# Kernel optimization log

Hardware: AMD Instinct MI355X
Metric: run time of the kernel (lower is better)

Reference implementation:

```python
import jax, jax.numpy as jnp
import numpy as np

B_, C_, T_, F_ = 1, 64, 256, 128
D_CONV, D_STATE, DT_RANK = 4, 16, 4
D_INNER = 2 * C_
EPS = 1e-5


def setup_inputs():
    key = jax.random.key(0)
    ks = jax.random.split(key, 12)
    s = 0.05
    return {
        'x': jax.random.normal(ks[0], (B_, C_, T_, F_), jnp.float32),
        'norm_w': jnp.ones((4, C_), jnp.float32),
        'in_proj_w': jax.random.normal(ks[1], (4, 2 * D_INNER, C_), jnp.float32) * s,
        'conv_w': jax.random.normal(ks[2], (4, D_INNER, 1, D_CONV), jnp.float32) * 0.3,
        'conv_b': jnp.zeros((4, D_INNER), jnp.float32),
        'x_proj_w': jax.random.normal(ks[3], (4, DT_RANK + 2 * D_STATE, D_INNER), jnp.float32) * s,
        'dt_proj_w': jax.random.normal(ks[4], (4, D_INNER, DT_RANK), jnp.float32) * 0.1,
        'dt_proj_b': jnp.log(jnp.expm1(jax.random.uniform(ks[5], (4, D_INNER), jnp.float32, 1e-3, 0.1))),
        'A_log': jnp.log(jax.random.uniform(ks[6], (4, D_INNER, D_STATE), jnp.float32, 0.5, 16.0)),
        'Dp': jnp.ones((4, D_INNER), jnp.float32),
        'out_proj_w': jax.random.normal(ks[7], (4, C_, D_INNER), jnp.float32) * s,
        'tlin_w': jax.random.normal(ks[8], (2 * C_, C_), jnp.float32) * s,
        'tlin_b': jnp.zeros((C_,), jnp.float32),
        'flin_w': jax.random.normal(ks[9], (2 * C_, C_), jnp.float32) * s,
        'flin_b': jnp.zeros((C_,), jnp.float32),
    }


def _rmsnorm(x, w):
    return x * jax.lax.rsqrt(jnp.mean(x * x, axis=-1, keepdims=True) + EPS) * w


def _mamba(u, p):
    # u: (N, L, d_model) ; selective-scan Mamba mixer
    N, L, _ = u.shape
    xz = jnp.einsum('nld,ed->nle', u, p['in_proj_w'])  # (N,L,2*di)
    x, z = jnp.split(xz, 2, axis=-1)
    # causal depthwise conv over time
    xT = jnp.swapaxes(x, 1, 2)  # (N, di, L)
    xc = jax.lax.conv_general_dilated(xT, p['conv_w'], (1,), [(D_CONV - 1, 0)],
                                      feature_group_count=D_INNER)
    x = jnp.swapaxes(jax.nn.silu(xc + p['conv_b'][None, :, None]), 1, 2)  # (N,L,di)
    xdbl = jnp.einsum('nld,ed->nle', x, p['x_proj_w'])
    dt, Bm, Cm = jnp.split(xdbl, [DT_RANK, DT_RANK + D_STATE], axis=-1)
    dt = jax.nn.softplus(jnp.einsum('nlr,dr->nld', dt, p['dt_proj_w']) + p['dt_proj_b'])
    A = -jnp.exp(p['A_log'])  # (di, ds)

    def step(h, inp):
        dt_t, B_t, C_t, x_t = inp  # (N,di),(N,ds),(N,ds),(N,di)
        dA = jnp.exp(dt_t[:, :, None] * A)  # (N,di,ds)
        h = dA * h + dt_t[:, :, None] * B_t[:, None, :] * x_t[:, :, None]
        return h, jnp.einsum('nds,ns->nd', h, C_t)

    h0 = jnp.zeros((N, D_INNER, D_STATE), u.dtype)
    _, ys = jax.lax.scan(step, h0, (jnp.swapaxes(dt, 0, 1), jnp.swapaxes(Bm, 0, 1),
                                    jnp.swapaxes(Cm, 0, 1), jnp.swapaxes(x, 0, 1)))
    y = jnp.swapaxes(ys, 0, 1) + x * p['Dp']
    y = y * jax.nn.silu(z)
    return jnp.einsum('nld,od->nlo', y, p['out_proj_w'])


def _block(u, p):
    # mamba Block with residual: out = mixer(rmsnorm(u)) + u
    return _mamba(_rmsnorm(u, p['norm_w']), p) + u


def _bimamba(u, pf, pb):
    yf = _block(u, pf)
    yb = jnp.flip(_block(jnp.flip(u, 1), pb), 1)
    return jnp.concatenate([yf, yb], axis=-1)


def _pick(i, norm_w, in_proj_w, conv_w, conv_b, x_proj_w, dt_proj_w, dt_proj_b, A_log, Dp, out_proj_w):
    return dict(norm_w=norm_w[i], in_proj_w=in_proj_w[i], conv_w=conv_w[i], conv_b=conv_b[i],
                x_proj_w=x_proj_w[i], dt_proj_w=dt_proj_w[i], dt_proj_b=dt_proj_b[i],
                A_log=A_log[i], Dp=Dp[i], out_proj_w=out_proj_w[i])


def _tfmamba(x, norm_w, in_proj_w, conv_w, conv_b, x_proj_w, dt_proj_w, dt_proj_b,
             A_log, Dp, out_proj_w, tlin_w, tlin_b, flin_w, flin_b):
    b, c, t, f = x.shape
    P = [_pick(i, norm_w, in_proj_w, conv_w, conv_b, x_proj_w, dt_proj_w, dt_proj_b, A_log, Dp, out_proj_w)
         for i in range(4)]
    # time axis
    xt = jnp.reshape(jnp.transpose(x, (0, 3, 2, 1)), (b * f, t, c))
    xt_out = _bimamba(xt, P[0], P[1])  # (b*f, t, 2c)
    xt = xt + jnp.einsum('nti,io->nto', xt_out, tlin_w) + tlin_b
    # frequency axis
    xf = jnp.reshape(jnp.transpose(jnp.reshape(xt, (b, f, t, c)), (0, 2, 1, 3)), (b * t, f, c))
    xf_out = _bimamba(xf, P[2], P[3])  # (b*t, f, 2c)
    xf = xf + jnp.einsum('nfi,io->nfo', xf_out, flin_w) + flin_b
    return jnp.transpose(jnp.reshape(xf, (b, t, f, c)), (0, 3, 1, 2))


def reference(x, norm_w, in_proj_w, conv_w, conv_b, x_proj_w, dt_proj_w, dt_proj_b,
              A_log, Dp, out_proj_w, tlin_w, tlin_b, flin_w, flin_b):
    return _tfmamba(x, norm_w, in_proj_w, conv_w, conv_b, x_proj_w, dt_proj_w, dt_proj_b,
                    A_log, Dp, out_proj_w, tlin_w, tlin_b, flin_w, flin_b)
```

## Files before the change

kernel.cpp:

```cpp
#include <hip/hip_runtime.h>
#include <math.h>

#define C_DIM 64
#define T_DIM 256
#define F_DIM 128
#define DI    128
#define DS    16
#define CK    16

typedef __attribute__((ext_vector_type(8))) short bf16x8;
typedef __attribute__((ext_vector_type(4))) float f32x4;

__device__ __forceinline__ float silu_f(float v){ return v / (1.0f + __expf(-v)); }

__device__ __forceinline__ unsigned short f2bf(float f){
  union{float f; unsigned u;} v; v.f = f;
  unsigned r = v.u + 0x7FFFu + ((v.u >> 16) & 1u);
  return (unsigned short)(r >> 16);
}

__device__ __forceinline__ int swz64(int row, int col){
  return row*64 + (col ^ ((row & 7) << 3));
}
__device__ __forceinline__ int swz128(int row, int col){
  return row*128 + (col ^ ((row & 7) << 3));
}

__global__ __launch_bounds__(256) void k_prep(const float* __restrict__ ipw,
                                              const float* __restrict__ opw,
                                              const float* __restrict__ xpw,
                                              const float* __restrict__ tlw,
                                              unsigned short* __restrict__ wbuf){
  const int i = blockIdx.x*256 + threadIdx.x;
  if(i < 65536){
    wbuf[i] = f2bf(ipw[i]);
  } else if(i < 98304){
    wbuf[i] = f2bf(opw[i - 65536]);
  } else if(i < 122880){
    const int j = i - 98304;
    const int p = j / 6144, rr = (j - p*6144) >> 7, k = j & 127;
    wbuf[i] = (rr < 36) ? f2bf(xpw[p*4608 + rr*128 + k]) : (unsigned short)0;
  } else {
    const int j = i - 122880;
    const int o = j >> 7, k = j & 127;
    wbuf[i] = f2bf(tlw[k*64 + o]);
  }
}

__global__ __launch_bounds__(256) void k_transpose_in(const float* __restrict__ x,
                                                      float* __restrict__ xt){
  __shared__ float tile[64][133];
  const int t = blockIdx.x;
  {
    const int fi = threadIdx.x & 127, cg = threadIdx.x >> 7;
    for(int c = cg*32; c < cg*32 + 32; ++c)
      tile[c][fi] = x[(size_t)c*32768 + (size_t)t*128 + fi];
  }
  __syncthreads();
  {
    const int ci = threadIdx.x & 63, fg = threadIdx.x >> 6;
    for(int f = fg*32; f < fg*32 + 32; ++f)
      xt[(size_t)f*16384 + (size_t)t*64 + ci] = tile[ci][f];
  }
}

__global__ __launch_bounds__(256, 3) void k_mamba(
    const float* __restrict__ src, int N, int L, long long sn, long long sl,
    int pbase,
    const float* __restrict__ norm_w,   const unsigned short* __restrict__ wbf,
    const float* __restrict__ conv_w,   const float* __restrict__ conv_b,
    const float* __restrict__ dt_proj_w,
    const float* __restrict__ dt_proj_b,const float* __restrict__ A_log,
    const float* __restrict__ Dp,       float* __restrict__ obuf)
{
  __shared__ __align__(16) unsigned short u_bf[CK*64];
  __shared__ float x_s[CK+3][132];
  __shared__ float z_s[CK][132];
  __shared__ float xc_s[CK][132];
  __shared__ __align__(16) unsigned short xc_bf[CK*128];
  __shared__ __align__(16) float dtr_s[CK][4];
  __shared__ __align__(16) float B_s[CK][20];
  __shared__ __align__(16) float C_s[CK][20];
  __shared__ __align__(16) unsigned short y_bf[CK*128];
  __shared__ float w_cv[512];
  __shared__ float b_cv[128];
  __shared__ float nw[64];

  const int tid = threadIdx.x;
  const int bid = blockIdx.x;
  const int dir = (bid >= N) ? 1 : 0;
  const int n   = dir ? (bid - N) : bid;
  const int p   = pbase + dir;

  const int lane = tid & 63;
  const int wv   = tid >> 6;
  const int fr   = lane & 15;
  const int fk   = (lane >> 4) << 3;

  for(int i = tid; i < 512; i += 256) w_cv[i] = conv_w[p*512 + i];
  if(tid < 128) b_cv[tid] = conv_b[p*128 + tid];
  if(tid < 64) nw[tid] = norm_w[p*64 + tid];
  for(int i = tid; i < 3*128; i += 256){ x_s[i >> 7][i & 127] = 0.0f; }

  const unsigned short* WinB  = wbf + (size_t)p*16384;
  const unsigned short* WoutB = wbf + 65536 + (size_t)p*8192;
  const unsigned short* XpB   = wbf + 98304 + (size_t)p*6144;
  bf16x8 aW[4][2];
  #pragma unroll
  for(int ot = 0; ot < 4; ++ot)
    #pragma unroll
    for(int kh = 0; kh < 2; ++kh)
      aW[ot][kh] = *(const bf16x8*)(WinB + (wv*64 + ot*16 + fr)*64 + kh*32 + fk);
  bf16x8 aO[4];
  #pragma unroll
  for(int kc = 0; kc < 4; ++kc)
    aO[kc] = *(const bf16x8*)(WoutB + (wv*16 + fr)*128 + kc*32 + fk);
  bf16x8 aXP[4];
  if(wv < 3){
    #pragma unroll
    for(int kc = 0; kc < 4; ++kc)
      aXP[kc] = *(const bf16x8*)(XpB + (wv*16 + fr)*128 + kc*32 + fk);
  }

  const int d_own = tid >> 1;
  const int sh    = (tid & 1) * 8;
  const int odd   = tid & 1;
  const float4 wdt4  = *(const float4*)(dt_proj_w + p*512 + d_own*4);
  const float  bdt_r = dt_proj_b[p*128 + d_own];
  const float  dvec_r= Dp[p*128 + d_own];
  float A_r[8], h[8];
  #pragma unroll
  for(int i = 0; i < 8; ++i){
    A_r[i] = -__expf(A_log[p*2048 + d_own*16 + sh + i]) * 1.44269504f;
    h[i] = 0.0f;
  }
  __syncthreads();

  for(int c0 = 0; c0 < L; c0 += CK){
    if(c0 > 0){
      for(int i = tid; i < 3*128; i += 256){
        int r = i >> 7, ch = i & 127;
        x_s[r][ch] = x_s[CK + r][ch];
      }
    }
    {
      const int g = tid >> 4, j = tid & 15, c4 = j*4;
      const int l = c0 + g;
      const int lo = dir ? (L - 1 - l) : l;
      const float4 v = *(const float4*)(src + (size_t)n*sn + (size_t)lo*sl + c4);
      float ssq = v.x*v.x + v.y*v.y + v.z*v.z + v.w*v.w;
      ssq += __shfl_xor(ssq, 1); ssq += __shfl_xor(ssq, 2);
      ssq += __shfl_xor(ssq, 4); ssq += __shfl_xor(ssq, 8);
      const float sc = rsqrtf(ssq * (1.0f/64.0f) + 1e-5f);
      ushort4 pk;
      pk.x = f2bf(v.x * sc * nw[c4+0]);
      pk.y = f2bf(v.y * sc * nw[c4+1]);
      pk.z = f2bf(v.z * sc * nw[c4+2]);
      pk.w = f2bf(v.w * sc * nw[c4+3]);
      *(ushort4*)&u_bf[swz64(g, c4)] = pk;
    }
    __syncthreads();

    {
      const bf16x8 b0 = *(const bf16x8*)&u_bf[swz64(fr, fk)];
      const bf16x8 b1 = *(const bf16x8*)&u_bf[swz64(fr, 32 + fk)];
      #pragma unroll
      for(int ot = 0; ot < 4; ++ot){
        f32x4 acc = {0.f, 0.f, 0.f, 0.f};
        acc = __builtin_amdgcn_mfma_f32_16x16x32_bf16(aW[ot][0], b0, acc, 0, 0, 0);
        acc = __builtin_amdgcn_mfma_f32_16x16x32_bf16(aW[ot][1], b1, acc, 0, 0, 0);
        const int ob = wv*64 + ot*16 + ((lane >> 4) << 2);
        if(wv < 2){
          #pragma unroll
          for(int r = 0; r < 4; ++r) x_s[3 + fr][ob + r] = acc[r];
        } else {
          #pragma unroll
          for(int r = 0; r < 4; ++r) z_s[fr][ob + r - 128] = acc[r];
        }
      }
    }
    __syncthreads();

    {
      const int g = tid >> 4, j = tid & 15;
      #pragma unroll
      for(int i = 0; i < 8; ++i){
        const int ch = j + 16*i;
        float a = b_cv[ch];
        a += w_cv[ch*4+0] * x_s[g+0][ch];
        a += w_cv[ch*4+1] * x_s[g+1][ch];
        a += w_cv[ch*4+2] * x_s[g+2][ch];
        a += w_cv[ch*4+3] * x_s[g+3][ch];
        const float s = silu_f(a);
        xc_s[g][ch] = s;
        xc_bf[swz128(g, ch)] = f2bf(s);
      }
    }
    __syncthreads();

    if(wv < 3){
      f32x4 acc = {0.f, 0.f, 0.f, 0.f};
      #pragma unroll
      for(int kc = 0; kc < 4; ++kc){
        const bf16x8 b = *(const bf16x8*)&xc_bf[swz128(fr, kc*32 + fk)];
        acc = __builtin_amdgcn_mfma_f32_16x16x32_bf16(aXP[kc], b, acc, 0, 0, 0);
      }
      const int ob36 = wv*16 + ((lane >> 4) << 2);
      #pragma unroll
      for(int r = 0; r < 4; ++r){
        const int o36 = ob36 + r;
        const float v = acc[r];
        if(o36 < 4)       dtr_s[fr][o36] = v;
        else if(o36 < 20) B_s[fr][o36 - 4] = v;
        else if(o36 < 36) C_s[fr][o36 - 20] = v;
      }
    }
    __syncthreads();

    {
      float my_dt[8];
      #pragma unroll
      for(int q = 0; q < 8; ++q){
        const int l = odd*8 + q;
        const float4 r4 = *(const float4*)&dtr_s[l][0];
        float a = bdt_r + wdt4.x*r4.x + wdt4.y*r4.y + wdt4.z*r4.z + wdt4.w*r4.w;
        my_dt[q] = fmaxf(a, 0.0f) + log1pf(__expf(-fabsf(a)));
      }
      float ot_dt[8];
      #pragma unroll
      for(int q = 0; q < 8; ++q) ot_dt[q] = __shfl_xor(my_dt[q], 1);
      #pragma unroll
      for(int l = 0; l < CK; ++l){
        const float dtv = ((l >> 3) == odd) ? my_dt[l & 7] : ot_dt[l & 7];
        const float xv  = xc_s[l][d_own];
        const float4 b0 = *(const float4*)&B_s[l][sh];
        const float4 b1 = *(const float4*)&B_s[l][sh + 4];
        const float4 g0 = *(const float4*)&C_s[l][sh];
        const float4 g1 = *(const float4*)&C_s[l][sh + 4];
        const float bb[8] = {b0.x,b0.y,b0.z,b0.w,b1.x,b1.y,b1.z,b1.w};
        const float cc[8] = {g0.x,g0.y,g0.z,g0.w,g1.x,g1.y,g1.z,g1.w};
        const float dx = dtv * xv;
        float yp = 0.0f;
        #pragma unroll
        for(int i = 0; i < 8; ++i){
          h[i] = exp2f(dtv * A_r[i]) * h[i] + dx * bb[i];
          yp += h[i] * cc[i];
        }
        const float yo = yp + __shfl_xor(yp, 1);
        if(odd == 0){
          const float zv = z_s[l][d_own];
          y_bf[swz128(l, d_own)] = f2bf((yo + xv * dvec_r) * silu_f(zv));
        }
      }
    }
    __syncthreads();

    {
      f32x4 acc = {0.f, 0.f, 0.f, 0.f};
      #pragma unroll
      for(int kc = 0; kc < 4; ++kc){
        const bf16x8 b = *(const bf16x8*)&y_bf[swz128(fr, kc*32 + fk)];
        acc = __builtin_amdgcn_mfma_f32_16x16x32_bf16(aO[kc], b, acc, 0, 0, 0);
      }
      const int o2 = wv*16 + ((lane >> 4) << 2);
      const int l = c0 + fr;
      const int lo = dir ? (L - 1 - l) : l;
      float4 st; st.x = acc[0]; st.y = acc[1]; st.z = acc[2]; st.w = acc[3];
      *(float4*)(obuf + ((size_t)dir*32768 + (size_t)n*L + lo)*64 + o2) = st;
    }
  }
}

__global__ __launch_bounds__(256) void k_comb_time(
    const float* __restrict__ xt, const float* __restrict__ obuf,
    const unsigned short* __restrict__ wbf, const float* __restrict__ tlin_b,
    float* __restrict__ xt2)
{
  __shared__ __align__(16) unsigned short in_bf[64][128];
  __shared__ float xs[64][72];
  const int tid = threadIdx.x;
  const int lane = tid & 63, wv = tid >> 6;
  const int fr = lane & 15, fk = (lane >> 4) << 3;
  const int tk0 = blockIdx.x*64;

  const unsigned short* TL = wbf + 122880;
  bf16x8 aT[4];
  #pragma unroll
  for(int kc = 0; kc < 4; ++kc)
    aT[kc] = *(const bf16x8*)(TL + (wv*16 + fr)*128 + kc*32 + fk);

  {
    const int tg = tid >> 2, q = tid & 3;
    #pragma unroll
    for(int s = 0; s < 4; ++s){
      const int c4 = q*16 + s*4;
      const float4 xv = *(const float4*)(xt   + ((size_t)tk0 + tg)*64 + c4);
      const float4 fv = *(const float4*)(obuf + ((size_t)tk0 + tg)*64 + c4);
      const float4 bv = *(const float4*)(obuf + ((size_t)32768 + tk0 + tg)*64 + c4);
      ushort4 pf, pb;
      pf.x = f2bf(fv.x + xv.x); pf.y = f2bf(fv.y + xv.y);
      pf.z = f2bf(fv.z + xv.z); pf.w = f2bf(fv.w + xv.w);
      pb.x = f2bf(bv.x + xv.x); pb.y = f2bf(bv.y + xv.y);
      pb.z = f2bf(bv.z + xv.z); pb.w = f2bf(bv.w + xv.w);
      *(ushort4*)&in_bf[tg][c4]      = pf;
      *(ushort4*)&in_bf[tg][64 + c4] = pb;
      *(float4*)&xs[tg][c4] = xv;
    }
  }
  __syncthreads();

  {
    const int ob = wv*16 + ((lane >> 4) << 2);
    const float4 tb = *(const float4*)(tlin_b + ob);
    const float tbr[4] = {tb.x, tb.y, tb.z, tb.w};
    #pragma unroll
    for(int tt = 0; tt < 4; ++tt){
      f32x4 acc = {0.f, 0.f, 0.f, 0.f};
      #pragma unroll
      for(int kc = 0; kc < 4; ++kc){
        const bf16x8 b = *(const bf16x8*)&in_bf[tt*16 + fr][kc*32 + fk];
        acc = __builtin_amdgcn_mfma_f32_16x16x32_bf16(aT[kc], b, acc, 0, 0, 0);
      }
      const int token = tt*16 + fr;
      #pragma unroll
      for(int r = 0; r < 4; ++r)
        xs[token][ob + r] += tbr[r] + acc[r];
    }
  }
  __syncthreads();

  {
    const int tg = tid >> 2, q = tid & 3;
    #pragma unroll
    for(int s = 0; s < 4; ++s){
      const int c4 = q*16 + s*4;
      *(float4*)(xt2 + ((size_t)tk0 + tg)*64 + c4) = *(const float4*)&xs[tg][c4];
    }
  }
}

__global__ __launch_bounds__(256) void k_final(
    const float* __restrict__ xt2, const float* __restrict__ obuf,
    const float* __restrict__ flin_w, const float* __restrict__ flin_b,
    float* __restrict__ out)
{
  __shared__ float res_s[128][68];
  const int t = blockIdx.x, tid = threadIdx.x;
  const int f = tid >> 1, half = tid & 1, cbase = half*32;

  const float4* xr = (const float4*)(xt2  + (size_t)f*16384 + (size_t)t*64);
  const float4* fr = (const float4*)(obuf + ((size_t)t*128 + f)*64);
  const float4* br = (const float4*)(obuf + ((size_t)32768 + (size_t)t*128 + f)*64);

  float res[32];
  {
    const float4* fb = (const float4*)(flin_b + cbase);
    #pragma unroll
    for(int q = 0; q < 8; ++q){
      const float4 xv = xr[(cbase >> 2) + q], b = fb[q];
      res[q*4+0] = xv.x + b.x; res[q*4+1] = xv.y + b.y;
      res[q*4+2] = xv.z + b.z; res[q*4+3] = xv.w + b.w;
    }
  }
  for(int i4 = 0; i4 < 16; ++i4){
    const float4 xv4 = xr[i4], of4 = fr[i4], ob4 = br[i4];
    const float af[4] = {of4.x + xv4.x, of4.y + xv4.y, of4.z + xv4.z, of4.w + xv4.w};
    const float ab[4] = {ob4.x + xv4.x, ob4.y + xv4.y, ob4.z + xv4.z, ob4.w + xv4.w};
    #pragma unroll
    for(int ii = 0; ii < 4; ++ii){
      const int i = i4*4 + ii;
      const float4* F0 = (const float4*)(flin_w + i*64 + cbase);
      const float4* F1 = (const float4*)(flin_w + (64 + i)*64 + cbase);
      #pragma unroll
      for(int q = 0; q < 8; ++q){
        const float4 w0 = F0[q], w1 = F1[q];
        res[q*4+0] += af[ii]*w0.x + ab[ii]*w1.x;
        res[q*4+1] += af[ii]*w0.y + ab[ii]*w1.y;
        res[q*4+2] += af[ii]*w0.z + ab[ii]*w1.z;
        res[q*4+3] += af[ii]*w0.w + ab[ii]*w1.w;
      }
    }
  }
  #pragma unroll
  for(int c = 0; c < 32; ++c) res_s[f][cbase + c] = res[c];
  __syncthreads();
  {
    const int fi = tid & 127, cq = tid >> 7;
    for(int c = cq*32; c < cq*32 + 32; ++c)
      out[(size_t)c*32768 + (size_t)t*128 + fi] = res_s[fi][c];
  }
}

extern "C" void kernel_launch(void* const* d_in, const int* in_sizes, int n_in,
                              void* d_out, int out_size, void* d_ws, size_t ws_size,
                              hipStream_t stream){
  (void)in_sizes; (void)n_in; (void)out_size; (void)ws_size;
  const float* x         = (const float*)d_in[0];
  const float* norm_w    = (const float*)d_in[1];
  const float* in_proj_w = (const float*)d_in[2];
  const float* conv_w    = (const float*)d_in[3];
  const float* conv_b    = (const float*)d_in[4];
  const float* x_proj_w  = (const float*)d_in[5];
  const float* dt_proj_w = (const float*)d_in[6];
  const float* dt_proj_b = (const float*)d_in[7];
  const float* A_log     = (const float*)d_in[8];
  const float* Dp        = (const float*)d_in[9];
  const float* out_proj_w= (const float*)d_in[10];
  const float* tlin_w    = (const float*)d_in[11];
  const float* tlin_b    = (const float*)d_in[12];
  const float* flin_w    = (const float*)d_in[13];
  const float* flin_b    = (const float*)d_in[14];
  float* out = (float*)d_out;

  float* xt_buf = (float*)d_ws;
  float* obuf   = xt_buf + (size_t)(1u << 21);
  float* xt2    = obuf   + (size_t)(1u << 22);

  unsigned short* wbf = (unsigned short*)d_out;

  hipLaunchKernelGGL(k_prep, dim3(512), dim3(256), 0, stream,
      in_proj_w, out_proj_w, x_proj_w, tlin_w, wbf);

  hipLaunchKernelGGL(k_transpose_in, dim3(256), dim3(256), 0, stream, x, xt_buf);

  hipLaunchKernelGGL(k_mamba, dim3(256), dim3(256), 0, stream,
      xt_buf, 128, 256, (long long)16384, (long long)64, 0,
      norm_w, wbf, conv_w, conv_b, dt_proj_w, dt_proj_b,
      A_log, Dp, obuf);

  hipLaunchKernelGGL(k_comb_time, dim3(512), dim3(256), 0, stream,
      xt_buf, obuf, wbf, tlin_b, xt2);

  hipLaunchKernelGGL(k_mamba, dim3(512), dim3(256), 0, stream,
      xt2, 256, 128, (long long)64, (long long)16384, 2,
      norm_w, wbf, conv_w, conv_b, dt_proj_w, dt_proj_b,
      A_log, Dp, obuf);

  hipLaunchKernelGGL(k_final, dim3(256), dim3(256), 0, stream,
      xt2, obuf, flin_w, flin_b, out);
}
```

Measured before the change: 447.6 us.

## Widen Mamba blocks to 512 threads, 32-token chunks, 4 lanes per channel

Doubles the chunk length to 32 tokens and the block to 512 threads, so each channel's 16-state scan is split across 4 lanes instead of 2. Each thread does less serial scan work per step, and chunks, and therefore barriers, are halved. Out-projection results are staged in shared memory reusing the z buffer, then written as coalesced float4 rows during the next chunk's prologue. The cost is more shuffles per step, more shared memory per block and higher register pressure under launch_bounds(512,4), which may reduce occupancy.

```diff
diff --git a/kernel.cpp b/kernel.cpp
--- a/kernel.cpp
+++ b/kernel.cpp
@@ -6,7 +6,7 @@
 #define F_DIM 128
 #define DI    128
 #define DS    16
-#define CK    16
+#define CK    32
 
 typedef __attribute__((ext_vector_type(8))) short bf16x8;
 typedef __attribute__((ext_vector_type(4))) float f32x4;
@@ -64,7 +64,7 @@
   }
 }
 
-__global__ __launch_bounds__(256, 3) void k_mamba(
+__global__ __launch_bounds__(512, 4) void k_mamba(
     const float* __restrict__ src, int N, int L, long long sn, long long sl,
     int pbase,
     const float* __restrict__ norm_w,   const unsigned short* __restrict__ wbf,
@@ -74,9 +74,9 @@
     const float* __restrict__ Dp,       float* __restrict__ obuf)
 {
   __shared__ __align__(16) unsigned short u_bf[CK*64];
-  __shared__ float x_s[CK+3][132];
-  __shared__ float z_s[CK][132];
-  __shared__ float xc_s[CK][132];
+  __shared__ __align__(16) float x_s[CK+3][132];
+  __shared__ __align__(16) float zy[CK][132];
+  __shared__ __align__(16) float xc_s[CK][132];
   __shared__ __align__(16) unsigned short xc_bf[CK*128];
   __shared__ __align__(16) float dtr_s[CK][4];
   __shared__ __align__(16) float B_s[CK][20];
@@ -97,40 +97,44 @@
   const int fr   = lane & 15;
   const int fk   = (lane >> 4) << 3;
 
-  for(int i = tid; i < 512; i += 256) w_cv[i] = conv_w[p*512 + i];
+  if(tid < 512) w_cv[tid] = conv_w[p*512 + tid];
   if(tid < 128) b_cv[tid] = conv_b[p*128 + tid];
-  if(tid < 64) nw[tid] = norm_w[p*64 + tid];
-  for(int i = tid; i < 3*128; i += 256){ x_s[i >> 7][i & 127] = 0.0f; }
+  if(tid < 64)  nw[tid]   = norm_w[p*64 + tid];
+  if(tid < 384) x_s[tid >> 7][tid & 127] = 0.0f;
 
   const unsigned short* WinB  = wbf + (size_t)p*16384;
   const unsigned short* WoutB = wbf + 65536 + (size_t)p*8192;
   const unsigned short* XpB   = wbf + 98304 + (size_t)p*6144;
-  bf16x8 aW[4][2];
+  bf16x8 aW[2][2];
   #pragma unroll
-  for(int ot = 0; ot < 4; ++ot)
+  for(int j = 0; j < 2; ++j)
     #pragma unroll
     for(int kh = 0; kh < 2; ++kh)
-      aW[ot][kh] = *(const bf16x8*)(WinB + (wv*64 + ot*16 + fr)*64 + kh*32 + fk);
+      aW[j][kh] = *(const bf16x8*)(WinB + ((2*wv + j)*16 + fr)*64 + kh*32 + fk);
   bf16x8 aO[4];
-  #pragma unroll
-  for(int kc = 0; kc < 4; ++kc)
-    aO[kc] = *(const bf16x8*)(WoutB + (wv*16 + fr)*128 + kc*32 + fk);
+  {
+    const int ot = wv >> 1;
+    #pragma unroll
+    for(int kc = 0; kc < 4; ++kc)
+      aO[kc] = *(const bf16x8*)(WoutB + (ot*16 + fr)*128 + kc*32 + fk);
+  }
   bf16x8 aXP[4];
-  if(wv < 3){
+  if(wv < 6){
+    const int ot3 = wv >> 1;
     #pragma unroll
     for(int kc = 0; kc < 4; ++kc)
-      aXP[kc] = *(const bf16x8*)(XpB + (wv*16 + fr)*128 + kc*32 + fk);
-  }
-
-  const int d_own = tid >> 1;
-  const int sh    = (tid & 1) * 8;
-  const int odd   = tid & 1;
+      aXP[kc] = *(const bf16x8*)(XpB + (ot3*16 + fr)*128 + kc*32 + fk);
+  }
+
+  const int d_own = tid >> 2;
+  const int q     = tid & 3;
+  const int sh    = q * 4;
   const float4 wdt4  = *(const float4*)(dt_proj_w + p*512 + d_own*4);
   const float  bdt_r = dt_proj_b[p*128 + d_own];
   const float  dvec_r= Dp[p*128 + d_own];
-  float A_r[8], h[8];
+  float A_r[4], h[4];
   #pragma unroll
-  for(int i = 0; i < 8; ++i){
+  for(int i = 0; i < 4; ++i){
     A_r[i] = -__expf(A_log[p*2048 + d_own*16 + sh + i]) * 1.44269504f;
     h[i] = 0.0f;
   }
@@ -138,10 +142,15 @@
 
   for(int c0 = 0; c0 < L; c0 += CK){
     if(c0 > 0){
-      for(int i = tid; i < 3*128; i += 256){
-        int r = i >> 7, ch = i & 127;
+      if(tid < 384){
+        const int r = tid >> 7, ch = tid & 127;
         x_s[r][ch] = x_s[CK + r][ch];
       }
+      const int token = tid >> 4, c4 = (tid & 15) * 4;
+      const int l = (c0 - CK) + token;
+      const int lo = dir ? (L - 1 - l) : l;
+      const float4 v = *(const float4*)&zy[token][c4];
+      *(float4*)(obuf + ((size_t)dir*32768 + (size_t)n*L + lo)*64 + c4) = v;
     }
     {
       const int g = tid >> 4, j = tid & 15, c4 = j*4;
@@ -162,20 +171,24 @@
     __syncthreads();
 
     {
-      const bf16x8 b0 = *(const bf16x8*)&u_bf[swz64(fr, fk)];
-      const bf16x8 b1 = *(const bf16x8*)&u_bf[swz64(fr, 32 + fk)];
-      #pragma unroll
-      for(int ot = 0; ot < 4; ++ot){
-        f32x4 acc = {0.f, 0.f, 0.f, 0.f};
-        acc = __builtin_amdgcn_mfma_f32_16x16x32_bf16(aW[ot][0], b0, acc, 0, 0, 0);
-        acc = __builtin_amdgcn_mfma_f32_16x16x32_bf16(aW[ot][1], b1, acc, 0, 0, 0);
-        const int ob = wv*64 + ot*16 + ((lane >> 4) << 2);
-        if(wv < 2){
-          #pragma unroll
-          for(int r = 0; r < 4; ++r) x_s[3 + fr][ob + r] = acc[r];
-        } else {
-          #pragma unroll
-          for(int r = 0; r < 4; ++r) z_s[fr][ob + r - 128] = acc[r];
+      #pragma unroll
+      for(int tt = 0; tt < 2; ++tt){
+        const bf16x8 b0 = *(const bf16x8*)&u_bf[swz64(tt*16 + fr, fk)];
+        const bf16x8 b1 = *(const bf16x8*)&u_bf[swz64(tt*16 + fr, 32 + fk)];
+        #pragma unroll
+        for(int j = 0; j < 2; ++j){
+          f32x4 acc = {0.f, 0.f, 0.f, 0.f};
+          acc = __builtin_amdgcn_mfma_f32_16x16x32_bf16(aW[j][0], b0, acc, 0, 0, 0);
+          acc = __builtin_amdgcn_mfma_f32_16x16x32_bf16(aW[j][1], b1, acc, 0, 0, 0);
+          const int o  = (2*wv + j)*16 + ((lane >> 4) << 2);
+          const int tk = tt*16 + fr;
+          if(wv < 4){
+            #pragma unroll
+            for(int r = 0; r < 4; ++r) x_s[3 + tk][o + r] = acc[r];
+          } else {
+            #pragma unroll
+            for(int r = 0; r < 4; ++r) zy[tk][o + r - 128] = acc[r];
+          }
         }
       }
     }
@@ -198,21 +211,23 @@
     }
     __syncthreads();
 
-    if(wv < 3){
+    if(wv < 6){
+      const int tt = wv & 1;
       f32x4 acc = {0.f, 0.f, 0.f, 0.f};
       #pragma unroll
       for(int kc = 0; kc < 4; ++kc){
-        const bf16x8 b = *(const bf16x8*)&xc_bf[swz128(fr, kc*32 + fk)];
+        const bf16x8 b = *(const bf16x8*)&xc_bf[swz128(tt*16 + fr, kc*32 + fk)];
         acc = __builtin_amdgcn_mfma_f32_16x16x32_bf16(aXP[kc], b, acc, 0, 0, 0);
       }
-      const int ob36 = wv*16 + ((lane >> 4) << 2);
+      const int ob36 = (wv >> 1)*16 + ((lane >> 4) << 2);
+      const int tk = tt*16 + fr;
       #pragma unroll
       for(int r = 0; r < 4; ++r){
         const int o36 = ob36 + r;
         const float v = acc[r];
-        if(o36 < 4)       dtr_s[fr][o36] = v;
-        else if(o36 < 20) B_s[fr][o36 - 4] = v;
-        else if(o36 < 36) C_s[fr][o36 - 20] = v;
+        if(o36 < 4)       dtr_s[tk][o36] = v;
+        else if(o36 < 20) B_s[tk][o36 - 4] = v;
+        else if(o36 < 36) C_s[tk][o36 - 20] = v;
       }
     }
     __syncthreads();
@@ -220,54 +235,59 @@
     {
       float my_dt[8];
       #pragma unroll
-      for(int q = 0; q < 8; ++q){
-        const int l = odd*8 + q;
+      for(int m = 0; m < 8; ++m){
+        const int l = q*8 + m;
         const float4 r4 = *(const float4*)&dtr_s[l][0];
         float a = bdt_r + wdt4.x*r4.x + wdt4.y*r4.y + wdt4.z*r4.z + wdt4.w*r4.w;
-        my_dt[q] = fmaxf(a, 0.0f) + log1pf(__expf(-fabsf(a)));
-      }
-      float ot_dt[8];
-      #pragma unroll
-      for(int q = 0; q < 8; ++q) ot_dt[q] = __shfl_xor(my_dt[q], 1);
+        my_dt[m] = fmaxf(a, 0.0f) + log1pf(__expf(-fabsf(a)));
+      }
+      const int gbase = lane & ~3;
       #pragma unroll
       for(int l = 0; l < CK; ++l){
-        const float dtv = ((l >> 3) == odd) ? my_dt[l & 7] : ot_dt[l & 7];
+        const float dtv = __shfl(my_dt[l & 7], gbase | (l >> 3));
         const float xv  = xc_s[l][d_own];
-        const float4 b0 = *(const float4*)&B_s[l][sh];
-        const float4 b1 = *(const float4*)&B_s[l][sh + 4];
-        const float4 g0 = *(const float4*)&C_s[l][sh];
-        const float4 g1 = *(const float4*)&C_s[l][sh + 4];
-        const float bb[8] = {b0.x,b0.y,b0.z,b0.w,b1.x,b1.y,b1.z,b1.w};
-        const float cc[8] = {g0.x,g0.y,g0.z,g0.w,g1.x,g1.y,g1.z,g1.w};
+        const float4 b4 = *(const float4*)&B_s[l][sh];
+        const float4 c4v= *(const float4*)&C_s[l][sh];
+        const float bb[4] = {b4.x, b4.y, b4.z, b4.w};
+        const float cc[4] = {c4v.x, c4v.y, c4v.z, c4v.w};
         const float dx = dtv * xv;
         float yp = 0.0f;
         #pragma unroll
-        for(int i = 0; i < 8; ++i){
+        for(int i = 0; i < 4; ++i){
           h[i] = exp2f(dtv * A_r[i]) * h[i] + dx * bb[i];
           yp += h[i] * cc[i];
         }
-        const float yo = yp + __shfl_xor(yp, 1);
-        if(odd == 0){
-          const float zv = z_s[l][d_own];
-          y_bf[swz128(l, d_own)] = f2bf((yo + xv * dvec_r) * silu_f(zv));
+        yp += __shfl_xor(yp, 1);
+        yp += __shfl_xor(yp, 2);
+        if(q == 0){
+          const float zv = zy[l][d_own];
+          y_bf[swz128(l, d_own)] = f2bf((yp + xv * dvec_r) * silu_f(zv));
         }
       }
     }
     __syncthreads();
 
     {
+      const int tt = wv & 1;
       f32x4 acc = {0.f, 0.f, 0.f, 0.f};
       #pragma unroll
       for(int kc = 0; kc < 4; ++kc){
-        const bf16x8 b = *(const bf16x8*)&y_bf[swz128(fr, kc*32 + fk)];
+        const bf16x8 b = *(const bf16x8*)&y_bf[swz128(tt*16 + fr, kc*32 + fk)];
         acc = __builtin_amdgcn_mfma_f32_16x16x32_bf16(aO[kc], b, acc, 0, 0, 0);
       }
-      const int o2 = wv*16 + ((lane >> 4) << 2);
-      const int l = c0 + fr;
-      const int lo = dir ? (L - 1 - l) : l;
-      float4 st; st.x = acc[0]; st.y = acc[1]; st.z = acc[2]; st.w = acc[3];
-      *(float4*)(obuf + ((size_t)dir*32768 + (size_t)n*L + lo)*64 + o2) = st;
-    }
+      const int o2 = (wv >> 1)*16 + ((lane >> 4) << 2);
+      const int tk = tt*16 + fr;
+      #pragma unroll
+      for(int r = 0; r < 4; ++r) zy[tk][o2 + r] = acc[r];
+    }
+    __syncthreads();
+  }
+  {
+    const int token = tid >> 4, c4 = (tid & 15) * 4;
+    const int l = (L - CK) + token;
+    const int lo = dir ? (L - 1 - l) : l;
+    const float4 v = *(const float4*)&zy[token][c4];
+    *(float4*)(obuf + ((size_t)dir*32768 + (size_t)n*L + lo)*64 + c4) = v;
   }
 }
 
@@ -423,7 +443,7 @@
 
   hipLaunchKernelGGL(k_transpose_in, dim3(256), dim3(256), 0, stream, x, xt_buf);
 
-  hipLaunchKernelGGL(k_mamba, dim3(256), dim3(256), 0, stream,
+  hipLaunchKernelGGL(k_mamba, dim3(256), dim3(512), 0, stream,
       xt_buf, 128, 256, (long long)16384, (long long)64, 0,
       norm_w, wbf, conv_w, conv_b, dt_proj_w, dt_proj_b,
       A_log, Dp, obuf);
@@ -431,7 +451,7 @@
   hipLaunchKernelGGL(k_comb_time, dim3(512), dim3(256), 0, stream,
       xt_buf, obuf, wbf, tlin_b, xt2);
 
-  hipLaunchKernelGGL(k_mamba, dim3(512), dim3(256), 0, stream,
+  hipLaunchKernelGGL(k_mamba, dim3(512), dim3(512), 0, stream,
       xt2, 256, 128, (long long)64, (long long)16384, 2,
       norm_w, wbf, conv_w, conv_b, dt_proj_w, dt_proj_b,
       A_log, Dp, obuf);
```

After: 476.4 us. 6.4% more time.
